# Performance work log

Measured on AMD Instinct MI355X. Metric: run time of the kernel, lower is better.

Reference implementation:

```python
import jax, jax.numpy as jnp
import numpy as np

B, L, D = 4, 8192, 512
H, G = 8, 4
DH = D // H      # head channels = 64
GC = D // G      # group channels = 128
KSZ = 5          # kernel = offset_range_factor
PAD = KSZ // 2   # = 2; applied to BOTH offset convs (second conv has k=1, pad=2 -> length L+4)


def conv1d(x, w, b, pad):
    # x: (N, Cin, L), w: (Cout, Cin, K) torch layout
    y = jax.lax.conv_general_dilated(x, w, (1,), [(pad, pad)],
                                     dimension_numbers=('NCH', 'OIH', 'NCH'))
    return y + b[None, :, None]


def setup_inputs() -> dict:
    key = jax.random.key(0)
    ks = jax.random.split(key, 9)
    s = 0.02
    p = lambda k, shape: jax.random.normal(k, shape, jnp.float32) * s
    return {
        'x': jax.random.normal(ks[0], (B, L, D), jnp.float32),
        'Wq': p(ks[1], (D, D)), 'bq': jnp.zeros((D,), jnp.float32),
        'Wk': p(ks[2], (D, D)), 'bk': jnp.zeros((D,), jnp.float32),
        'Wv': p(ks[3], (D, D)), 'bv': jnp.zeros((D,), jnp.float32),
        'Woff1': p(ks[4], (GC, GC, KSZ)), 'boff1': jnp.zeros((GC,), jnp.float32),
        'Woff2': p(ks[5], (1, GC, 1)), 'boff2': jnp.zeros((1,), jnp.float32),
        'rel_bias': p(ks[6], (1, D, L)),
        'Wout': p(ks[7], (D, D)), 'bout': jnp.zeros((D,), jnp.float32),
    }


def reference(x, Wq, bq, Wk, bk, Wv, bv, Woff1, boff1, Woff2, boff2, rel_bias, Wout, bout):
    Bv, Lv, Dv = x.shape
    xc = jnp.transpose(x, (0, 2, 1))                         # (B, D, L)
    # 1x1 convs == pointwise linear over channels
    q = jnp.einsum('od,bdl->bol', Wq, xc) + bq[None, :, None]
    # offset prediction on grouped queries
    gq = q.reshape(Bv * G, GC, Lv)                            # (BG, GC, L)
    o = conv1d(gq, Woff1, boff1, PAD)                         # (BG, GC, L)
    o = conv1d(o, Woff2, boff2, PAD)                          # (BG, 1, L+4) due to k=1,pad=2
    offset = jnp.tanh(o[:, 0, :]) * KSZ                       # (BG, L+4)
    n = offset.shape[-1]
    vgrid = jnp.arange(n, dtype=x.dtype) + offset             # (BG, L+4)
    g = 2.0 * vgrid / (n - 1) - 1.0                           # normalized to [-1, 1] over n
    # torch grid_sample, align_corners=False, padding_mode='zeros', H = L
    pos = ((g + 1.0) * Lv - 1.0) / 2.0
    p0 = jnp.floor(pos)
    w1 = pos - p0                                             # weight for upper neighbor
    p0i = p0.astype(jnp.int32)
    p1i = p0i + 1
    feats = xc.reshape(Bv * G, GC, Lv)

    def gather(idx):
        valid = ((idx >= 0) & (idx < Lv)).astype(x.dtype)      # (BG, n)
        idxc = jnp.clip(idx, 0, Lv - 1)
        vals = jnp.take_along_axis(feats, idxc[:, None, :].astype(jnp.int32).repeat(1, axis=1), axis=2) if False else jnp.take_along_axis(feats, jnp.broadcast_to(idxc[:, None, :], (Bv * G, GC, n)), axis=2)
        return vals * valid[:, None, :]

    samp = gather(p0i) * (1.0 - w1)[:, None, :] + gather(p1i) * w1[:, None, :]
    x_sampled = samp[:, :, :Lv].reshape(Bv, Dv, Lv)           # (B, D, L)
    k = jnp.einsum('od,bdl->bol', Wk, x_sampled) + bk[None, :, None]
    v = jnp.einsum('od,bdl->bol', Wv, x_sampled) + bv[None, :, None] + rel_bias
    qh = q.reshape(Bv * H, DH, Lv)
    kh = k.reshape(Bv * H, DH, Lv)
    vh = v.reshape(Bv * H, DH, Lv)
    # channel-attention: contraction over sequence length L
    scores = jnp.einsum('bil,bjl->bij', qh, kh) * (Dv ** -0.5)  # (B*H, DH, DH)
    attn = jax.nn.softmax(scores, axis=-1)
    out = jnp.einsum('bij,bjl->bil', attn, vh)                # (B*H, DH, L)
    # rearrange '(b g) l c -> b c (g l)' with b=B, g=H, l=DH, c=L -> (B, L, D)
    out = jnp.transpose(out.reshape(Bv, H, DH, Lv), (0, 3, 1, 2)).reshape(Bv, Lv, H * DH)
    return out @ Wout.T + bout
```

## Files before the change

kernel.cpp:

```cpp
#include <hip/hip_runtime.h>
#include <hip/hip_bf16.h>
#include <math.h>

using u16 = unsigned short;
using u32 = unsigned int;

typedef __attribute__((ext_vector_type(8))) short s16x8;
typedef __attribute__((ext_vector_type(4))) float f32x4;

#define B_  4
#define L_  8192
#define D_  512
#define H_  8
#define G_  4

__device__ __forceinline__ float bf2f(u16 u) {
    u32 x = ((u32)u) << 16;
    return __uint_as_float(x);
}
__device__ __forceinline__ u16 f2bf(float f) {
    u32 x = __float_as_uint(f);
    u32 lsb = (x >> 16) & 1u;
    x += 0x7FFFu + lsb;
    return (u16)(x >> 16);
}
__device__ __forceinline__ void async16(const void* g, void* l) {
    __builtin_amdgcn_global_load_lds((const __attribute__((address_space(1))) u32*)g,
                                     (__attribute__((address_space(3))) u32*)l, 16, 0, 0);
}

__global__ __launch_bounds__(256) void cast_f32_bf16(const float* __restrict__ src,
                                                     u16* __restrict__ dst, int n4) {
    int i = blockIdx.x * 256 + threadIdx.x;
    if (i >= n4) return;
    float4 v = ((const float4*)src)[i];
    ushort4 o;
    o.x = f2bf(v.x); o.y = f2bf(v.y); o.z = f2bf(v.z); o.w = f2bf(v.w);
    ((ushort4*)dst)[i] = o;
}

__global__ __launch_bounds__(128) void build_weff(const float* __restrict__ W1,
                                                  const float* __restrict__ b1,
                                                  const float* __restrict__ W2,
                                                  const float* __restrict__ b2,
                                                  float* __restrict__ weff) {
    int idx = blockIdx.x * 128 + threadIdx.x;
    if (idx < 640) {
        int cin = idx / 5, dk = idx % 5;
        float acc = 0.f;
        for (int c = 0; c < 128; ++c) acc += W2[c] * W1[(c * 128 + cin) * 5 + dk];
        weff[idx] = acc;
    } else if (idx == 640) {
        float s = b2[0];
        for (int c = 0; c < 128; ++c) s += W2[c] * b1[c];
        weff[640] = s;
    } else if (idx == 641) {
        weff[641] = b2[0];
    }
}

__global__ __launch_bounds__(256) void offsets_kernel(const u16* __restrict__ qT,
                                                      const float* __restrict__ weff,
                                                      int* __restrict__ p0o,
                                                      float* __restrict__ w1o) {
    __shared__ u16 qs[128 * 72];
    __shared__ float wf[642];
    __shared__ float red[4][64];
    const int tid = threadIdx.x;
    const int t0 = blockIdx.x * 64;
    const int bg = blockIdx.y;
    const int b = bg >> 2, g = bg & 3;
    for (int i = tid; i < 642; i += 256) wf[i] = weff[i];
    for (int i = tid; i < 128 * 9; i += 256) {
        const int ch = i / 9, seg = i - ch * 9;
        const int l = t0 - 8 + seg * 8;
        s16x8 val = {0, 0, 0, 0, 0, 0, 0, 0};
        if (l >= 0)
            val = *(const s16x8*)(qT + (size_t)(b * D_ + g * 128 + ch) * L_ + l);
        *(s16x8*)(qs + ch * 72 + seg * 8) = val;
    }
    __syncthreads();
    const int w = tid >> 6, lane = tid & 63;
    float acc = 0.f;
    for (int c = 0; c < 32; ++c) {
        const int ch = w * 32 + c;
        const u16* row = qs + ch * 72 + lane + 4;
        const float* wr = wf + ch * 5;
        #pragma unroll
        for (int dk = 0; dk < 5; ++dk) acc += wr[dk] * bf2f(row[dk]);
    }
    red[w][lane] = acc;
    __syncthreads();
    if (w == 0) {
        const float s = red[0][lane] + red[1][lane] + red[2][lane] + red[3][lane];
        const int t = t0 + lane;
        const float o2 = (t >= 2) ? (s + wf[640]) : wf[641];
        const double offv = tanh((double)o2) * 5.0;
        const double vg  = (double)t + offv;
        const double gg  = 2.0 * vg / 8195.0 - 1.0;
        const double pos = ((gg + 1.0) * 8192.0 - 1.0) * 0.5;
        const double p0d = floor(pos);
        p0o[(size_t)bg * L_ + t] = (int)p0d;
        w1o[(size_t)bg * L_ + t] = (float)(pos - p0d);
    }
}

__global__ __launch_bounds__(256) void sample_kernel(const float* __restrict__ x,
                                                     const int* __restrict__ p0i,
                                                     const float* __restrict__ w1f,
                                                     u16* __restrict__ xs) {
    const size_t idx = (size_t)blockIdx.x * 256 + threadIdx.x;
    const int d = (int)(idx & 511);
    const int t = (int)((idx >> 9) & 8191);
    const int b = (int)(idx >> 22);
    const int g = d >> 7;
    const size_t og = (size_t)(b * 4 + g) * L_ + t;
    const int p0 = p0i[og];
    const float w1 = w1f[og];
    const int p1 = p0 + 1;
    float v0 = (p0 >= 0 && p0 < L_) ? x[((size_t)b * L_ + p0) * D_ + d] : 0.f;
    float v1 = (p1 >= 0 && p1 < L_) ? x[((size_t)b * L_ + p1) * D_ + d] : 0.f;
    xs[idx] = f2bf(v0 * (1.f - w1) + v1 * w1);
}

template <int MODE>
__global__ __launch_bounds__(256) void gemm_kernel(const u16* __restrict__ A,
                                                   const u16* __restrict__ W,
                                                   const float* __restrict__ bias,
                                                   const float* __restrict__ rel,
                                                   void* __restrict__ out) {
    __shared__ short As[128 * 32];
    __shared__ short Bs[128 * 32];
    const int tid = threadIdx.x;
    const int wave = tid >> 6, lane = tid & 63;
    const int r0 = blockIdx.y * 128;
    const int c0 = blockIdx.x * 128;
    const u16* Wb = (MODE == 2) ? (W + (size_t)(r0 >> 13) * D_ * D_) : W;
    const int wm = (wave >> 1) * 64, wn = (wave & 1) * 64;
    const int srow = lane >> 2;
    const int scol = (lane & 3) * 8;

    f32x4 acc[4][4];
    #pragma unroll
    for (int mi = 0; mi < 4; ++mi)
        #pragma unroll
        for (int ni = 0; ni < 4; ++ni) acc[mi][ni] = (f32x4){0.f, 0.f, 0.f, 0.f};

    for (int k0 = 0; k0 < D_; k0 += 32) {
        #pragma unroll
        for (int i = 0; i < 2; ++i) {
            const int rr = wave * 32 + i * 16 + srow;
            const u16* ga = A  + (size_t)(r0 + rr) * D_ + k0 + scol;
            const u16* gb = Wb + (size_t)(c0 + rr) * D_ + k0 + scol;
            async16(ga, &As[(wave * 32 + i * 16) * 32]);
            async16(gb, &Bs[(wave * 32 + i * 16) * 32]);
        }
        __syncthreads();
        const int fm = lane & 15;
        const int kq = (lane >> 4) * 8;
        s16x8 af[4], bfr[4];
        #pragma unroll
        for (int mi = 0; mi < 4; ++mi) af[mi]  = *(const s16x8*)(As + (wm + mi * 16 + fm) * 32 + kq);
        #pragma unroll
        for (int ni = 0; ni < 4; ++ni) bfr[ni] = *(const s16x8*)(Bs + (wn + ni * 16 + fm) * 32 + kq);
        #pragma unroll
        for (int mi = 0; mi < 4; ++mi)
            #pragma unroll
            for (int ni = 0; ni < 4; ++ni)
                acc[mi][ni] = __builtin_amdgcn_mfma_f32_16x16x32_bf16(af[mi], bfr[ni], acc[mi][ni], 0, 0, 0);
        __syncthreads();
    }
    const int fn = lane & 15;
    const int q4 = (lane >> 4) * 4;
    #pragma unroll
    for (int mi = 0; mi < 4; ++mi) {
        #pragma unroll
        for (int ni = 0; ni < 4; ++ni) {
            const int c = c0 + wn + ni * 16 + fn;
            const float bsum = bias[c];
            if (MODE == 0) {
                const int r_ = r0 + wm + mi * 16 + q4;
                const int bb = r_ >> 13;
                const int l  = r_ & (L_ - 1);
                ushort4 o;
                o.x = f2bf(acc[mi][ni][0] + bsum);
                o.y = f2bf(acc[mi][ni][1] + bsum);
                o.z = f2bf(acc[mi][ni][2] + bsum);
                o.w = f2bf(acc[mi][ni][3] + bsum);
                *(ushort4*)((u16*)out + (size_t)(bb * D_ + c) * L_ + l) = o;
            } else {
                #pragma unroll
                for (int rg = 0; rg < 4; ++rg) {
                    const int r = r0 + wm + mi * 16 + q4 + rg;
                    float v = acc[mi][ni][rg] + bsum;
                    if (MODE == 1) v += rel[(size_t)c * L_ + (r & (L_ - 1))];
                    if (MODE == 2) ((float*)out)[(size_t)r * D_ + c] = v;
                    else           ((u16*)out)[(size_t)r * D_ + c] = f2bf(v);
                }
            }
        }
    }
}

__global__ __launch_bounds__(256) void scores_partial(const u16* __restrict__ qT,
                                                      const u16* __restrict__ kT,
                                                      float* __restrict__ part) {
    __shared__ u16 qs[64 * 136];
    __shared__ u16 ks[64 * 136];
    const int chunk = blockIdx.x;
    const int bh = blockIdx.y;
    const int b = bh >> 3, h = bh & 7;
    const int tid = threadIdx.x;
    const int wave = tid >> 6, lane = tid & 63;
    const int wr = (wave >> 1) * 32;
    const int wc = (wave & 1) * 32;
    f32x4 acc[2][2];
    #pragma unroll
    for (int mi = 0; mi < 2; ++mi)
        #pragma unroll
        for (int ni = 0; ni < 2; ++ni) acc[mi][ni] = (f32x4){0.f, 0.f, 0.f, 0.f};
    const size_t base = (size_t)(b * D_ + h * 64) * L_;
    const int m = lane & 15, q = lane >> 4;
    for (int iter = 0; iter < 4; ++iter) {
        const int l0 = chunk * 512 + iter * 128;
        __syncthreads();
        for (int i = tid; i < 1024; i += 256) {
            const int lb = i & 15, ch = i >> 4;
            const size_t gidx = base + (size_t)ch * L_ + l0 + lb * 8;
            *(s16x8*)(qs + ch * 136 + lb * 8) = *(const s16x8*)(qT + gidx);
            *(s16x8*)(ks + ch * 136 + lb * 8) = *(const s16x8*)(kT + gidx);
        }
        __syncthreads();
        #pragma unroll
        for (int kst = 0; kst < 4; ++kst) {
            const int kk = kst * 32 + q * 8;
            s16x8 af[2], bfr[2];
            af[0]  = *(const s16x8*)(qs + (wr + m) * 136 + kk);
            af[1]  = *(const s16x8*)(qs + (wr + 16 + m) * 136 + kk);
            bfr[0] = *(const s16x8*)(ks + (wc + m) * 136 + kk);
            bfr[1] = *(const s16x8*)(ks + (wc + 16 + m) * 136 + kk);
            #pragma unroll
            for (int mi = 0; mi < 2; ++mi)
                #pragma unroll
                for (int ni = 0; ni < 2; ++ni)
                    acc[mi][ni] = __builtin_amdgcn_mfma_f32_16x16x32_bf16(af[mi], bfr[ni], acc[mi][ni], 0, 0, 0);
        }
    }
    float* dst = part + (size_t)(bh * 16 + chunk) * 4096;
    const int q4 = (lane >> 4) * 4;
    #pragma unroll
    for (int mi = 0; mi < 2; ++mi) {
        #pragma unroll
        for (int ni = 0; ni < 2; ++ni) {
            const int j = wc + ni * 16 + m;
            #pragma unroll
            for (int rg = 0; rg < 4; ++rg) {
                const int i = wr + mi * 16 + q4 + rg;
                dst[i * 64 + j] = acc[mi][ni][rg];
            }
        }
    }
}

__global__ __launch_bounds__(256) void softmax_kernel(const float* __restrict__ part,
                                                      float* __restrict__ attn) {
    const int tid = threadIdx.x;
    const int wave = tid >> 6, lane = tid & 63;
    const int row = blockIdx.x * 4 + wave;
    const int bh = row >> 6, i = row & 63;
    float s = 0.f;
    #pragma unroll
    for (int c = 0; c < 16; ++c) s += part[((size_t)(bh * 16 + c)) * 4096 + i * 64 + lane];
    s *= 0.04419417382415922f;
    float m = s;
    for (int off = 32; off > 0; off >>= 1) m = fmaxf(m, __shfl_xor(m, off));
    float e = expf(s - m);
    float sum = e;
    for (int off = 32; off > 0; off >>= 1) sum += __shfl_xor(sum, off);
    attn[(size_t)bh * 4096 + i * 64 + lane] = e / sum;
}

__global__ __launch_bounds__(256) void build_M(const float* __restrict__ Wout,
                                               const float* __restrict__ attn,
                                               u16* __restrict__ M) {
    const int idx = blockIdx.x * 256 + threadIdx.x;
    const int col = idx & 511;
    const int o = (idx >> 9) & 511;
    const int b = idx >> 18;
    const int h = col >> 6, j = col & 63;
    const float* wr = Wout + o * 512 + h * 64;
    const float* ar = attn + (size_t)(b * H_ + h) * 4096 + j;
    float s = 0.f;
    #pragma unroll 8
    for (int i = 0; i < 64; ++i) s += wr[i] * ar[i * 64];
    M[idx] = f2bf(s);
}

extern "C" void kernel_launch(void* const* d_in, const int* in_sizes, int n_in,
                              void* d_out, int out_size, void* d_ws, size_t ws_size,
                              hipStream_t stream) {
    const float* x    = (const float*)d_in[0];
    const float* Wq   = (const float*)d_in[1];
    const float* bq   = (const float*)d_in[2];
    const float* Wk   = (const float*)d_in[3];
    const float* bk   = (const float*)d_in[4];
    const float* Wv   = (const float*)d_in[5];
    const float* bv   = (const float*)d_in[6];
    const float* Wo1  = (const float*)d_in[7];
    const float* bo1  = (const float*)d_in[8];
    const float* Wo2  = (const float*)d_in[9];
    const float* bo2  = (const float*)d_in[10];
    const float* rel  = (const float*)d_in[11];
    const float* Wout = (const float*)d_in[12];
    const float* bout = (const float*)d_in[13];

    char* ws = (char*)d_ws;
    const size_t MB = 1024ull * 1024ull;
    u16*   x_bf  = (u16*)(ws);
    u16*   qT    = (u16*)(ws + 32 * MB);
    u16*   kT    = (u16*)(ws + 64 * MB);
    u16*   v_bf  = (u16*)(ws + 96 * MB);
    u16*   wq_bf = (u16*)(ws + 128 * MB);
    u16*   wk_bf = wq_bf + 262144;
    u16*   wv_bf = wk_bf + 262144;
    float* weff  = (float*)(ws + 130 * MB);
    int*   p0i   = (int*)(ws + 130 * MB + 65536);
    float* w1f   = (float*)((char*)p0i + 524288);
    float* part  = (float*)((char*)w1f + 524288);
    float* attn  = (float*)((char*)part + 8 * MB);
    u16*   M_bf  = (u16*)((char*)attn + 524288);

    cast_f32_bf16<<<16384, 256, 0, stream>>>(x, x_bf, 4194304);
    cast_f32_bf16<<<256, 256, 0, stream>>>(Wq, wq_bf, 65536);
    cast_f32_bf16<<<256, 256, 0, stream>>>(Wk, wk_bf, 65536);
    cast_f32_bf16<<<256, 256, 0, stream>>>(Wv, wv_bf, 65536);
    build_weff<<<6, 128, 0, stream>>>(Wo1, bo1, Wo2, bo2, weff);
    gemm_kernel<0><<<dim3(4, 256), 256, 0, stream>>>(x_bf, wq_bf, bq, nullptr, (void*)qT);
    offsets_kernel<<<dim3(128, 16), 256, 0, stream>>>(qT, weff, p0i, w1f);
    sample_kernel<<<65536, 256, 0, stream>>>(x, p0i, w1f, x_bf);
    gemm_kernel<0><<<dim3(4, 256), 256, 0, stream>>>(x_bf, wk_bf, bk, nullptr, (void*)kT);
    gemm_kernel<1><<<dim3(4, 256), 256, 0, stream>>>(x_bf, wv_bf, bv, rel, (void*)v_bf);
    scores_partial<<<dim3(16, 32), 256, 0, stream>>>(qT, kT, part);
    softmax_kernel<<<512, 256, 0, stream>>>(part, attn);
    build_M<<<4096, 256, 0, stream>>>(Wout, attn, M_bf);
    gemm_kernel<2><<<dim3(4, 256), 256, 0, stream>>>(v_bf, M_bf, bout, nullptr, d_out);
}
```

Baseline: 435.9 us.

## Vectorize sampling loads, swizzle GEMM LDS tiles, remap blocks for XCD locality

The sample kernel now has each thread handle four channels. It uses float4 loads and a packed ushort4 store, which cuts the thread count and the number of memory transactions. The GEMM kernel XOR-swizzles the 16-byte column chunks in shared memory on both the async store and the fragment read side, to reduce LDS bank conflicts. It also uses a 1D grid whose block index is remapped so that consecutive row tiles land on the same XCD for better L2 reuse. The swizzle must match between the async write address and the read address, or the result will be wrong.

New measurement: 409.3 us. 1.06x faster.

```diff
diff --git a/kernel.cpp b/kernel.cpp
--- a/kernel.cpp
+++ b/kernel.cpp
@@ -109,18 +109,25 @@
                                                      const int* __restrict__ p0i,
                                                      const float* __restrict__ w1f,
                                                      u16* __restrict__ xs) {
-    const size_t idx = (size_t)blockIdx.x * 256 + threadIdx.x;
-    const int d = (int)(idx & 511);
-    const int t = (int)((idx >> 9) & 8191);
-    const int b = (int)(idx >> 22);
-    const int g = d >> 7;
+    const size_t idx4 = (size_t)blockIdx.x * 256 + threadIdx.x;
+    const int d4 = (int)(idx4 & 127);
+    const int t = (int)((idx4 >> 7) & 8191);
+    const int b = (int)(idx4 >> 20);
+    const int g = d4 >> 5;
     const size_t og = (size_t)(b * 4 + g) * L_ + t;
     const int p0 = p0i[og];
     const float w1 = w1f[og];
+    const float w0 = 1.f - w1;
     const int p1 = p0 + 1;
-    float v0 = (p0 >= 0 && p0 < L_) ? x[((size_t)b * L_ + p0) * D_ + d] : 0.f;
-    float v1 = (p1 >= 0 && p1 < L_) ? x[((size_t)b * L_ + p1) * D_ + d] : 0.f;
-    xs[idx] = f2bf(v0 * (1.f - w1) + v1 * w1);
+    float4 v0 = {0.f, 0.f, 0.f, 0.f}, v1 = {0.f, 0.f, 0.f, 0.f};
+    if (p0 >= 0 && p0 < L_) v0 = *(const float4*)(x + ((size_t)b * L_ + p0) * D_ + d4 * 4);
+    if (p1 >= 0 && p1 < L_) v1 = *(const float4*)(x + ((size_t)b * L_ + p1) * D_ + d4 * 4);
+    ushort4 o;
+    o.x = f2bf(v0.x * w0 + v1.x * w1);
+    o.y = f2bf(v0.y * w0 + v1.y * w1);
+    o.z = f2bf(v0.z * w0 + v1.z * w1);
+    o.w = f2bf(v0.w * w0 + v1.w * w1);
+    ((ushort4*)xs)[idx4] = o;
 }
 
 template <int MODE>
@@ -133,18 +140,25 @@
     __shared__ short Bs[128 * 32];
     const int tid = threadIdx.x;
     const int wave = tid >> 6, lane = tid & 63;
-    const int r0 = blockIdx.y * 128;
-    const int c0 = blockIdx.x * 128;
+    const int bid = blockIdx.x;
+    const int xcd = bid & 7;
+    const int kk_ = bid >> 3;
+    const int r0 = (xcd * 32 + (kk_ >> 2)) * 128;
+    const int c0 = (kk_ & 3) * 128;
     const u16* Wb = (MODE == 2) ? (W + (size_t)(r0 >> 13) * D_ * D_) : W;
     const int wm = (wave >> 1) * 64, wn = (wave & 1) * 64;
     const int srow = lane >> 2;
-    const int scol = (lane & 3) * 8;
+    const int gcb  = (lane & 3) ^ ((srow >> 1) & 3);
+    const int scol = gcb * 8;
 
     f32x4 acc[4][4];
     #pragma unroll
     for (int mi = 0; mi < 4; ++mi)
         #pragma unroll
         for (int ni = 0; ni < 4; ++ni) acc[mi][ni] = (f32x4){0.f, 0.f, 0.f, 0.f};
+
+    const int fm = lane & 15;
+    const int sblk = ((lane >> 4) ^ ((fm >> 1) & 3)) * 8;
 
     for (int k0 = 0; k0 < D_; k0 += 32) {
         #pragma unroll
@@ -156,13 +170,11 @@
             async16(gb, &Bs[(wave * 32 + i * 16) * 32]);
         }
         __syncthreads();
-        const int fm = lane & 15;
-        const int kq = (lane >> 4) * 8;
         s16x8 af[4], bfr[4];
         #pragma unroll
-        for (int mi = 0; mi < 4; ++mi) af[mi]  = *(const s16x8*)(As + (wm + mi * 16 + fm) * 32 + kq);
-        #pragma unroll
-        for (int ni = 0; ni < 4; ++ni) bfr[ni] = *(const s16x8*)(Bs + (wn + ni * 16 + fm) * 32 + kq);
+        for (int mi = 0; mi < 4; ++mi) af[mi]  = *(const s16x8*)(As + (wm + mi * 16 + fm) * 32 + sblk);
+        #pragma unroll
+        for (int ni = 0; ni < 4; ++ni) bfr[ni] = *(const s16x8*)(Bs + (wn + ni * 16 + fm) * 32 + sblk);
         #pragma unroll
         for (int mi = 0; mi < 4; ++mi)
             #pragma unroll
@@ -335,13 +347,13 @@
     cast_f32_bf16<<<256, 256, 0, stream>>>(Wk, wk_bf, 65536);
     cast_f32_bf16<<<256, 256, 0, stream>>>(Wv, wv_bf, 65536);
     build_weff<<<6, 128, 0, stream>>>(Wo1, bo1, Wo2, bo2, weff);
-    gemm_kernel<0><<<dim3(4, 256), 256, 0, stream>>>(x_bf, wq_bf, bq, nullptr, (void*)qT);
+    gemm_kernel<0><<<1024, 256, 0, stream>>>(x_bf, wq_bf, bq, nullptr, (void*)qT);
     offsets_kernel<<<dim3(128, 16), 256, 0, stream>>>(qT, weff, p0i, w1f);
-    sample_kernel<<<65536, 256, 0, stream>>>(x, p0i, w1f, x_bf);
-    gemm_kernel<0><<<dim3(4, 256), 256, 0, stream>>>(x_bf, wk_bf, bk, nullptr, (void*)kT);
-    gemm_kernel<1><<<dim3(4, 256), 256, 0, stream>>>(x_bf, wv_bf, bv, rel, (void*)v_bf);
+    sample_kernel<<<16384, 256, 0, stream>>>(x, p0i, w1f, x_bf);
+    gemm_kernel<0><<<1024, 256, 0, stream>>>(x_bf, wk_bf, bk, nullptr, (void*)kT);
+    gemm_kernel<1><<<1024, 256, 0, stream>>>(x_bf, wv_bf, bv, rel, (void*)v_bf);
     scores_partial<<<dim3(16, 32), 256, 0, stream>>>(qT, kT, part);
     softmax_kernel<<<512, 256, 0, stream>>>(part, attn);
     build_M<<<4096, 256, 0, stream>>>(Wout, attn, M_bf);
-    gemm_kernel<2><<<dim3(4, 256), 256, 0, stream>>>(v_bf, M_bf, bout, nullptr, d_out);
-}
+    gemm_kernel<2><<<1024, 256, 0, stream>>>(v_bf, M_bf, bout, nullptr, d_out);
+}
```
